# Optimization experiments

Hardware: AMD Instinct MI355X
Metric: run time of the kernel (lower is better)

The kernel has to match this reference:

```python
import jax, jax.numpy as jnp
import numpy as np
import math

C = 512
B, T = 8, 2048
STRIDE = 2
LN_EPS = 1e-5
EPS = 1e-8


def _ln(x, g, b):
    mu = jnp.mean(x, axis=-1, keepdims=True)
    var = jnp.mean(jnp.square(x - mu), axis=-1, keepdims=True)
    return (x - mu) * jax.lax.rsqrt(var + LN_EPS) * g + b


def _lin(x, w, b):
    # torch Linear: y = x @ W^T + b, W: [out, in]
    return jnp.einsum('btc,oc->bto', x, w) + b


def setup_inputs() -> dict:
    key = jax.random.key(0)
    ks = iter(jax.random.split(key, 40))
    s = 0.02
    d = {'x': jax.random.normal(next(ks), (B, T, C), jnp.float32)}
    # downsample conv: [C_out, C_in, K]
    d['dw'] = jax.random.normal(next(ks), (C, C, 3), jnp.float32) * s
    d['db'] = jnp.zeros((C,), jnp.float32)
    for br in ('cr', 'd', 'c'):
        for p in ('q', 'k', 'v'):
            d[f'w{p}_{br}'] = jax.random.normal(next(ks), (C, C), jnp.float32) * s
            d[f'b{p}_{br}'] = jnp.zeros((C,), jnp.float32)
        d[f'ln_{br}_g'] = jnp.ones((C,), jnp.float32)
        d[f'ln_{br}_b'] = jnp.zeros((C,), jnp.float32)
    d['temp'] = jnp.asarray(0.1, jnp.float32)
    d['gw'] = jax.random.normal(next(ks), (3, 3 * C), jnp.float32) * s  # conv1d k=1 squeezed
    d['gb'] = jnp.zeros((3,), jnp.float32)
    return d


def _forward(x, dw, db, wq_cr, bq_cr, wk_cr, bk_cr, wv_cr, bv_cr, ln_cr_g, ln_cr_b,
             wq_d, bq_d, wk_d, bk_d, wv_d, bv_d, ln_d_g, ln_d_b,
             wq_c, bq_c, wk_c, bk_c, wv_c, bv_c, ln_c_g, ln_c_b,
             temp, gw, gb):
    scale = 1.0 / math.sqrt(C)
    # downsample: Conv1d(k=3, stride, pad=1) on [B,C,T]
    xc = jnp.transpose(x, (0, 2, 1))
    xd = jax.lax.conv_general_dilated(
        xc, dw, window_strides=(STRIDE,), padding=[(1, 1)],
        dimension_numbers=('NCH', 'OIH', 'NCH')) + db[None, :, None]
    x_down = jnp.transpose(xd, (0, 2, 1))  # [B, T//2, C]

    # cross-resolution branch
    q = _lin(x, wq_cr, bq_cr)
    k = _lin(x_down, wk_cr, bk_cr)
    v = _lin(x_down, wv_cr, bv_cr)
    a = jax.nn.softmax(jnp.einsum('btc,bsc->bts', q, k) * scale, axis=-1)
    out_cross = _ln(jnp.einsum('bts,bsc->btc', a, v), ln_cr_g, ln_cr_b)

    # dot-product branch
    q = _lin(x, wq_d, bq_d)
    k = _lin(x, wk_d, bk_d)
    v = _lin(x, wv_d, bv_d)
    a = jax.nn.softmax(jnp.einsum('btc,bsc->bts', q, k) * scale, axis=-1)
    out_dot = _ln(jnp.einsum('bts,bsc->btc', a, v), ln_d_g, ln_d_b)

    # cosine branch with learnable temperature
    q = _lin(x, wq_c, bq_c)
    k = _lin(x, wk_c, bk_c)
    qn = q / (jnp.linalg.norm(q, axis=2, keepdims=True) + EPS)
    kn = k / (jnp.linalg.norm(k, axis=2, keepdims=True) + EPS)
    t = jnp.maximum(temp, 0.01)
    a = jax.nn.softmax(jnp.einsum('btc,bsc->bts', qn, kn) / t, axis=-1)
    v = _lin(x, wv_c, bv_c)
    out_cos = _ln(jnp.einsum('bts,bsc->btc', a, v), ln_c_g, ln_c_b)

    # learned gating fusion (conv1d k=1 == per-position linear over 3C)
    fused = jnp.concatenate([out_cross, out_dot, out_cos], axis=-1)  # [B,T,3C]
    gate = jax.nn.softmax(jnp.einsum('btc,gc->btg', fused, gw) + gb, axis=-1)  # [B,T,3]
    z = (gate[..., 0:1] * out_cross + gate[..., 1:2] * out_dot + gate[..., 2:3] * out_cos)
    return z


def reference(x, dw, db, wq_cr, bq_cr, wk_cr, bk_cr, wv_cr, bv_cr, ln_cr_g, ln_cr_b,
              wq_d, bq_d, wk_d, bk_d, wv_d, bv_d, ln_d_g, ln_d_b,
              wq_c, bq_c, wk_c, bk_c, wv_c, bv_c, ln_c_g, ln_c_b,
              temp, gw, gb):
    return _forward(x, dw, db, wq_cr, bq_cr, wk_cr, bk_cr, wv_cr, bv_cr, ln_cr_g, ln_cr_b,
                    wq_d, bq_d, wk_d, bk_d, wv_d, bv_d, ln_d_g, ln_d_b,
                    wq_c, bq_c, wk_c, bk_c, wv_c, bv_c, ln_c_g, ln_c_b,
                    temp, gw, gb)
```

## Files before the change

kernel.cpp:

```cpp
#include <hip/hip_runtime.h>


typedef __attribute__((ext_vector_type(8))) __bf16 bf16x8;
typedef __attribute__((ext_vector_type(4))) float f32x4;

#define CDIM 512
#define TFULL 2048

#define GLL16(gp, lp)                                                        \
  __builtin_amdgcn_global_load_lds(                                          \
      (const __attribute__((address_space(1))) unsigned int*)(gp),           \
      (__attribute__((address_space(3))) unsigned int*)(lp), 16, 0, 0)

__device__ __forceinline__ unsigned short f2bf(float f) {
  unsigned u = __float_as_uint(f);
  u = (u + 0x7fffu + ((u >> 16) & 1u)) >> 16;
  return (unsigned short)u;
}
__device__ __forceinline__ float bf2f(unsigned short h) {
  return __uint_as_float(((unsigned)h) << 16);
}

__global__ __launch_bounds__(256)
void k_tobf16(const float* __restrict__ src, unsigned short* __restrict__ dst, long n4) {
  long i = (long)blockIdx.x * 256 + threadIdx.x;
  if (i >= n4) return;
  float4 f = reinterpret_cast<const float4*>(src)[i];
  unsigned short o4[4] = {f2bf(f.x), f2bf(f.y), f2bf(f.z), f2bf(f.w)};
  reinterpret_cast<uint2*>(dst)[i] = *reinterpret_cast<const uint2*>(o4);
}

struct WPtrs { const float* p[9]; };
__global__ __launch_bounds__(256)
void k_tobf16w(WPtrs w, unsigned short* __restrict__ dst) {
  int idx = blockIdx.x * 256 + threadIdx.x;
  if (idx >= 9 * 65536) return;
  int m = idx >> 16, off = idx & 65535;
  float4 f = reinterpret_cast<const float4*>(w.p[m])[off];
  unsigned short o4[4] = {f2bf(f.x), f2bf(f.y), f2bf(f.z), f2bf(f.w)};
  reinterpret_cast<uint2*>(dst + (long)m * 262144)[off] = *reinterpret_cast<const uint2*>(o4);
}

__global__ __launch_bounds__(256)
void k_dwreorder(const float* __restrict__ dw, unsigned short* __restrict__ dwb) {
  int idx = blockIdx.x * 256 + threadIdx.x;
  if (idx >= 512 * 1536) return;
  int o = idx / 1536, rem = idx - o * 1536;
  int k = rem >> 9, i = rem & 511;
  dwb[idx] = f2bf(dw[(o * 512 + i) * 3 + k]);
}

__global__ __launch_bounds__(256)
void k_fix(const unsigned short* __restrict__ XB, const unsigned short* __restrict__ DWB,
           const float* __restrict__ db, unsigned short* __restrict__ XD) {
  const int lane = threadIdx.x & 63, wave = threadIdx.x >> 6;
  const int idx = blockIdx.x * 4 + wave;
  const int b = idx >> 9, o = idx & 511;
  const unsigned short* xr = XB + (long)b * TFULL * CDIM + lane * 16;
  const unsigned short* wr = DWB + (long)o * 1536 + 512 + lane * 16;
  float acc = 0.f;
  uint4 xv0 = *reinterpret_cast<const uint4*>(xr);
  uint4 xv1 = *reinterpret_cast<const uint4*>(xr + 8);
  uint4 wv0 = *reinterpret_cast<const uint4*>(wr);
  uint4 wv1 = *reinterpret_cast<const uint4*>(wr + 8);
  const unsigned short* xp0 = (const unsigned short*)&xv0;
  const unsigned short* xp1 = (const unsigned short*)&xv1;
  const unsigned short* wp0 = (const unsigned short*)&wv0;
  const unsigned short* wp1 = (const unsigned short*)&wv1;
#pragma unroll
  for (int j = 0; j < 8; ++j) acc += bf2f(xp0[j]) * bf2f(wp0[j]);
#pragma unroll
  for (int j = 0; j < 8; ++j) acc += bf2f(xp1[j]) * bf2f(wp1[j]);
#pragma unroll
  for (int off = 32; off > 0; off >>= 1) acc += __shfl_xor(acc, off);
  if (lane == 0) XD[(long)b * 1024 * 512 + o] = f2bf(acc + db[o]);
}

__global__ __launch_bounds__(256)
void k_gemm(const unsigned short* __restrict__ A,
            const unsigned short* __restrict__ B,
            void* __restrict__ Cp,
            int K, int lda, int ldb, int ldc,
            long sA, long sB, long sC,
            const float* __restrict__ bias,
            float alpha, int mode) {
  const int gx = gridDim.x;
  const int nwg = gx * gridDim.y;
  int wg = blockIdx.x + gx * blockIdx.y;
  wg = (wg & 7) * (nwg >> 3) + (wg >> 3);
  const int tm0 = (wg % gx) * 128, tn0 = (wg / gx) * 128;
  const int bz = blockIdx.z;
  const unsigned short* Ag = A + (long)bz * sA;
  const unsigned short* Bg = B + (long)bz * sB;

  __shared__ __align__(16) unsigned short smem[32768];

  const int tid = threadIdx.x;
  const int lane = tid & 63;
  const int wave = tid >> 6;
  const int wm = (wave >> 1) * 64, wn = (wave & 1) * 64;
  const int lrow = lane & 15, kq = lane >> 4;

  f32x4 acc[4][4];
#pragma unroll
  for (int i = 0; i < 4; ++i)
#pragma unroll
    for (int j = 0; j < 4; ++j) acc[i][j] = f32x4{0.f, 0.f, 0.f, 0.f};

  const int sr = tid >> 3;
  const int sj = (tid & 7) ^ (sr & 7);
  const unsigned short* aSrc = Ag + (long)(tm0 + sr) * lda + sj * 8;
  const unsigned short* bSrc = Bg + (long)(tn0 + sr) * ldb + sj * 8;

  const int nt = K >> 6;

#define STAGE(kt_, buf_)                                                     \
  {                                                                          \
    unsigned short* aD = smem + (buf_) * 8192 + wave * 512;                  \
    unsigned short* bD = smem + 16384 + (buf_) * 8192 + wave * 512;          \
    _Pragma("unroll")                                                        \
    for (int rd = 0; rd < 4; ++rd) {                                         \
      GLL16(aSrc + (kt_) + (long)rd * 32 * lda, aD + rd * 2048);             \
      GLL16(bSrc + (kt_) + (long)rd * 32 * ldb, bD + rd * 2048);             \
    }                                                                        \
  }

  STAGE(0, 0);

  const int xr = (lrow & 7) << 3;
  for (int t = 0; t < nt; ++t) {
    if (t + 1 < nt) {
      STAGE((t + 1) << 6, (t + 1) & 1);
      asm volatile("s_waitcnt vmcnt(8)" ::: "memory");
    } else {
      asm volatile("s_waitcnt vmcnt(0)" ::: "memory");
    }
    __builtin_amdgcn_s_barrier();
    __builtin_amdgcn_sched_barrier(0);
    const unsigned short* As_ = smem + (t & 1) * 8192;
    const unsigned short* Bs_ = smem + 16384 + (t & 1) * 8192;
    bf16x8 af[4][2], bfv[4][2];
#pragma unroll
    for (int mi = 0; mi < 4; ++mi)
#pragma unroll
      for (int ks = 0; ks < 2; ++ks)
        af[mi][ks] = *reinterpret_cast<const bf16x8*>(
            &As_[(wm + mi * 16 + lrow) * 64 + ((ks * 32 + kq * 8) ^ xr)]);
#pragma unroll
    for (int ni = 0; ni < 4; ++ni)
#pragma unroll
      for (int ks = 0; ks < 2; ++ks)
        bfv[ni][ks] = *reinterpret_cast<const bf16x8*>(
            &Bs_[(wn + ni * 16 + lrow) * 64 + ((ks * 32 + kq * 8) ^ xr)]);
#pragma unroll
    for (int mi = 0; mi < 4; ++mi)
#pragma unroll
      for (int ni = 0; ni < 4; ++ni) {
        acc[mi][ni] = __builtin_amdgcn_mfma_f32_16x16x32_bf16(af[mi][0], bfv[ni][0], acc[mi][ni], 0, 0, 0);
        acc[mi][ni] = __builtin_amdgcn_mfma_f32_16x16x32_bf16(af[mi][1], bfv[ni][1], acc[mi][ni], 0, 0, 0);
      }
    __builtin_amdgcn_sched_barrier(0);
    if (t + 1 < nt) __builtin_amdgcn_s_barrier();
  }
#undef STAGE

  unsigned short* Cb = (unsigned short*)Cp + (long)bz * sC;
  if (mode == 1) {
#pragma unroll
    for (int mi = 0; mi < 4; ++mi) {
      int rg = tm0 + wm + mi * 16 + kq * 4;
#pragma unroll
      for (int ni = 0; ni < 4; ++ni) {
        int cg = tn0 + wn + ni * 16 + lrow;
        float bb = bias ? bias[cg] : 0.f;
        f32x4 v = acc[mi][ni];
#pragma unroll
        for (int r = 0; r < 4; ++r)
          Cb[(long)(rg + r) * ldc + cg] = f2bf(v[r] * alpha + bb);
      }
    }
  } else {
#pragma unroll
    for (int mi = 0; mi < 4; ++mi) {
      int rg = tm0 + wm + mi * 16 + kq * 4;
      float rb[4];
#pragma unroll
      for (int r = 0; r < 4; ++r) rb[r] = bias[rg + r];
#pragma unroll
      for (int ni = 0; ni < 4; ++ni) {
        int cg = tn0 + wn + ni * 16 + lrow;
        f32x4 v = acc[mi][ni];
#pragma unroll
        for (int r = 0; r < 4; ++r)
          Cb[(long)(rg + r) * ldc + cg] = f2bf(v[r] * alpha + rb[r]);
      }
    }
  }
}

__global__ __launch_bounds__(256)
void k_gemm64(const unsigned short* __restrict__ A,
              const unsigned short* __restrict__ B,
              void* __restrict__ Cp,
              int K, int lda, int ldb, int ldc,
              long sA, long sB, long sC,
              const float* __restrict__ bias,
              float alpha, int mode) {
  const int gx = gridDim.x;
  const int nwg = gx * gridDim.y;
  int wg = blockIdx.x + gx * blockIdx.y;
  wg = (wg & 7) * (nwg >> 3) + (wg >> 3);
  const int tm0 = (wg % gx) * 128, tn0 = (wg / gx) * 64;
  const int bz = blockIdx.z;
  const unsigned short* Ag = A + (long)bz * sA;
  const unsigned short* Bg = B + (long)bz * sB;

  __shared__ __align__(16) unsigned short smem[24576];

  const int tid = threadIdx.x;
  const int lane = tid & 63;
  const int wave = tid >> 6;
  const int wm = (wave >> 1) * 64, wn = (wave & 1) * 32;
  const int lrow = lane & 15, kq = lane >> 4;

  f32x4 acc[4][2];
#pragma unroll
  for (int i = 0; i < 4; ++i)
#pragma unroll
    for (int j = 0; j < 2; ++j) acc[i][j] = f32x4{0.f, 0.f, 0.f, 0.f};

  const int sr = tid >> 3;
  const int sj = (tid & 7) ^ (sr & 7);
  const unsigned short* aSrc = Ag + (long)(tm0 + sr) * lda + sj * 8;
  const unsigned short* bSrc = Bg + (long)(tn0 + sr) * ldb + sj * 8;

  const int nt = K >> 6;

#define STAGE64(kt_, buf_)                                                   \
  {                                                                          \
    unsigned short* aD = smem + (buf_) * 8192 + wave * 512;                  \
    unsigned short* bD = smem + 16384 + (buf_) * 4096 + wave * 512;          \
    _Pragma("unroll")                                                        \
    for (int rd = 0; rd < 4; ++rd)                                           \
      GLL16(aSrc + (kt_) + (long)rd * 32 * lda, aD + rd * 2048);             \
    _Pragma("unroll")                                                        \
    for (int rd = 0; rd < 2; ++rd)                                           \
      GLL16(bSrc + (kt_) + (long)rd * 32 * ldb, bD + rd * 2048);             \
  }

  STAGE64(0, 0);

  const int xr = (lrow & 7) << 3;
  for (int t = 0; t < nt; ++t) {
    if (t + 1 < nt) {
      STAGE64((t + 1) << 6, (t + 1) & 1);
      asm volatile("s_waitcnt vmcnt(6)" ::: "memory");
    } else {
      asm volatile("s_waitcnt vmcnt(0)" ::: "memory");
    }
    __builtin_amdgcn_s_barrier();
    __builtin_amdgcn_sched_barrier(0);
    const unsigned short* As_ = smem + (t & 1) * 8192;
    const unsigned short* Bs_ = smem + 16384 + (t & 1) * 4096;
    bf16x8 af[4][2], bfv[2][2];
#pragma unroll
    for (int mi = 0; mi < 4; ++mi)
#pragma unroll
      for (int ks = 0; ks < 2; ++ks)
        af[mi][ks] = *reinterpret_cast<const bf16x8*>(
            &As_[(wm + mi * 16 + lrow) * 64 + ((ks * 32 + kq * 8) ^ xr)]);
#pragma unroll
    for (int ni = 0; ni < 2; ++ni)
#pragma unroll
      for (int ks = 0; ks < 2; ++ks)
        bfv[ni][ks] = *reinterpret_cast<const bf16x8*>(
            &Bs_[(wn + ni * 16 + lrow) * 64 + ((ks * 32 + kq * 8) ^ xr)]);
#pragma unroll
    for (int mi = 0; mi < 4; ++mi)
#pragma unroll
      for (int ni = 0; ni < 2; ++ni) {
        acc[mi][ni] = __builtin_amdgcn_mfma_f32_16x16x32_bf16(af[mi][0], bfv[ni][0], acc[mi][ni], 0, 0, 0);
        acc[mi][ni] = __builtin_amdgcn_mfma_f32_16x16x32_bf16(af[mi][1], bfv[ni][1], acc[mi][ni], 0, 0, 0);
      }
    __builtin_amdgcn_sched_barrier(0);
    if (t + 1 < nt) __builtin_amdgcn_s_barrier();
  }
#undef STAGE64

  unsigned short* Cb = (unsigned short*)Cp + (long)bz * sC;
  if (mode == 1) {
#pragma unroll
    for (int mi = 0; mi < 4; ++mi) {
      int rg = tm0 + wm + mi * 16 + kq * 4;
#pragma unroll
      for (int ni = 0; ni < 2; ++ni) {
        int cg = tn0 + wn + ni * 16 + lrow;
        float bb = bias ? bias[cg] : 0.f;
        f32x4 v = acc[mi][ni];
#pragma unroll
        for (int r = 0; r < 4; ++r)
          Cb[(long)(rg + r) * ldc + cg] = f2bf(v[r] * alpha + bb);
      }
    }
  } else {
#pragma unroll
    for (int mi = 0; mi < 4; ++mi) {
      int rg = tm0 + wm + mi * 16 + kq * 4;
      float rb[4];
#pragma unroll
      for (int r = 0; r < 4; ++r) rb[r] = bias[rg + r];
#pragma unroll
      for (int ni = 0; ni < 2; ++ni) {
        int cg = tn0 + wn + ni * 16 + lrow;
        f32x4 v = acc[mi][ni];
#pragma unroll
        for (int r = 0; r < 4; ++r)
          Cb[(long)(rg + r) * ldc + cg] = f2bf(v[r] * alpha + rb[r]);
      }
    }
  }
}

__global__ __launch_bounds__(512)
void k_gemm256(const unsigned short* __restrict__ A,
               const unsigned short* __restrict__ B,
               unsigned short* __restrict__ C,
               int K, int lda, int ldb, int ldc,
               long sA, long sB, long sC,
               float alpha, const float* __restrict__ tempPtr) {
  const int gx = gridDim.x;
  const int nwg = gx * gridDim.y;
  int wg = blockIdx.x + gx * blockIdx.y;
  wg = (wg & 7) * (nwg >> 3) + (wg >> 3);
  const int tm0 = (wg % gx) * 256, tn0 = (wg / gx) * 256;
  const unsigned short* Ag = A + (long)blockIdx.z * sA;
  const unsigned short* Bg = B + (long)blockIdx.z * sB;

  __shared__ __align__(16) unsigned short smem[32768];

  const int tid = threadIdx.x;
  const int lane = tid & 63;
  const int wave = tid >> 6;
  const int wm = (wave >> 2) * 128, wn = (wave & 3) * 64;
  const int lrow = lane & 15, kq = lane >> 4;

  f32x4 acc[8][4];
#pragma unroll
  for (int i = 0; i < 8; ++i)
#pragma unroll
    for (int j = 0; j < 4; ++j) acc[i][j] = f32x4{0.f, 0.f, 0.f, 0.f};

  const int srow = lane >> 2;
  const int sslot = (lane & 3) ^ ((lane >> 3) & 3);
  const unsigned short* aS0 = Ag + (long)(tm0 + wave * 16 + srow) * lda + sslot * 8;
  const unsigned short* aS1 = aS0 + 128L * lda;
  const unsigned short* bS0 = Bg + (long)(tn0 + wave * 16 + srow) * ldb + sslot * 8;
  const unsigned short* bS1 = bS0 + 128L * ldb;

  const int nt = K >> 5;

#define STAGE256(kt_, buf_)                                                  \
  {                                                                          \
    unsigned short* aD = smem + (buf_) * 8192 + wave * 512;                  \
    unsigned short* bD = smem + 16384 + (buf_) * 8192 + wave * 512;          \
    GLL16(aS0 + (kt_), aD);                                                  \
    GLL16(aS1 + (kt_), aD + 4096);                                           \
    GLL16(bS0 + (kt_), bD);                                                  \
    GLL16(bS1 + (kt_), bD + 4096);                                           \
  }

  STAGE256(0, 0);

  const int xr = ((lrow >> 1) & 3) << 3;
  for (int t = 0; t < nt; ++t) {
    if (t + 1 < nt) {
      STAGE256((t + 1) << 5, (t + 1) & 1);
      asm volatile("s_waitcnt vmcnt(4)" ::: "memory");
    } else {
      asm volatile("s_waitcnt vmcnt(0)" ::: "memory");
    }
    __builtin_amdgcn_s_barrier();
    __builtin_amdgcn_sched_barrier(0);
    const unsigned short* As_ = smem + (t & 1) * 8192;
    const unsigned short* Bs_ = smem + 16384 + (t & 1) * 8192;
    bf16x8 bfv[4];
#pragma unroll
    for (int ni = 0; ni < 4; ++ni)
      bfv[ni] = *reinterpret_cast<const bf16x8*>(
          &Bs_[(wn + ni * 16 + lrow) * 32 + ((kq * 8) ^ xr)]);
#pragma unroll
    for (int mi = 0; mi < 8; ++mi) {
      bf16x8 af = *reinterpret_cast<const bf16x8*>(
          &As_[(wm + mi * 16 + lrow) * 32 + ((kq * 8) ^ xr)]);
#pragma unroll
      for (int ni = 0; ni < 4; ++ni)
        acc[mi][ni] = __builtin_amdgcn_mfma_f32_16x16x32_bf16(af, bfv[ni], acc[mi][ni], 0, 0, 0);
    }
    __builtin_amdgcn_sched_barrier(0);
    if (t + 1 < nt) __builtin_amdgcn_s_barrier();
  }
#undef STAGE256

  if (tempPtr) alpha = 1.0f / fmaxf(*tempPtr, 0.01f);

  C += (long)blockIdx.z * sC;
#pragma unroll
  for (int mi = 0; mi < 8; ++mi) {
    int rg = tm0 + wm + mi * 16 + kq * 4;
#pragma unroll
    for (int ni = 0; ni < 4; ++ni) {
      int cg = tn0 + wn + ni * 16 + lrow;
      f32x4 v = acc[mi][ni];
#pragma unroll
      for (int r = 0; r < 4; ++r)
        C[(long)(rg + r) * ldc + cg] = f2bf(v[r] * alpha);
    }
  }
}

__global__ __launch_bounds__(256)
void k_softmax(unsigned short* __restrict__ S, int cols) {
  const long base = (long)blockIdx.x * cols;
  const int tid = threadIdx.x, lane = tid & 63, wave = tid >> 6;
  const int nv = cols >> 3;
  float f[8];
  float mx = -3.0e38f;
  if (tid < nv) {
    uint4 v = *reinterpret_cast<const uint4*>(S + base + tid * 8);
    const unsigned short* pv = (const unsigned short*)&v;
#pragma unroll
    for (int j = 0; j < 8; ++j) { f[j] = bf2f(pv[j]); mx = fmaxf(mx, f[j]); }
  }
  __shared__ float rmax[4], rsum[4];
#pragma unroll
  for (int o = 32; o > 0; o >>= 1) mx = fmaxf(mx, __shfl_down(mx, o));
  if (lane == 0) rmax[wave] = mx;
  __syncthreads();
  mx = fmaxf(fmaxf(rmax[0], rmax[1]), fmaxf(rmax[2], rmax[3]));
  float sum = 0.f;
  if (tid < nv) {
#pragma unroll
    for (int j = 0; j < 8; ++j) { f[j] = __expf(f[j] - mx); sum += f[j]; }
  }
#pragma unroll
  for (int o = 32; o > 0; o >>= 1) sum += __shfl_down(sum, o);
  if (lane == 0) rsum[wave] = sum;
  __syncthreads();
  const float inv = 1.0f / (rsum[0] + rsum[1] + rsum[2] + rsum[3]);
  if (tid < nv) {
    unsigned short o8[8];
#pragma unroll
    for (int j = 0; j < 8; ++j) o8[j] = f2bf(f[j] * inv);
    *reinterpret_cast<uint4*>(S + base + tid * 8) = *reinterpret_cast<const uint4*>(o8);
  }
}

__global__ __launch_bounds__(256)
void k_softmax1024(unsigned short* __restrict__ S) {
  const int tid = threadIdx.x;
  const int half = tid >> 7, ht = tid & 127;
  const int lane = tid & 63, wave = tid >> 6;
  const long base = ((long)blockIdx.x * 2 + half) * 1024;
  uint4 v = *reinterpret_cast<const uint4*>(S + base + ht * 8);
  const unsigned short* pv = (const unsigned short*)&v;
  float f[8];
  float mx = -3.0e38f;
#pragma unroll
  for (int j = 0; j < 8; ++j) { f[j] = bf2f(pv[j]); mx = fmaxf(mx, f[j]); }
  __shared__ float rmax[4], rsum[4];
#pragma unroll
  for (int o = 32; o > 0; o >>= 1) mx = fmaxf(mx, __shfl_down(mx, o));
  if (lane == 0) rmax[wave] = mx;
  __syncthreads();
  mx = fmaxf(rmax[half * 2], rmax[half * 2 + 1]);
  float sum = 0.f;
#pragma unroll
  for (int j = 0; j < 8; ++j) { f[j] = __expf(f[j] - mx); sum += f[j]; }
#pragma unroll
  for (int o = 32; o > 0; o >>= 1) sum += __shfl_down(sum, o);
  if (lane == 0) rsum[wave] = sum;
  __syncthreads();
  const float inv = 1.0f / (rsum[half * 2] + rsum[half * 2 + 1]);
  unsigned short o8[8];
#pragma unroll
  for (int j = 0; j < 8; ++j) o8[j] = f2bf(f[j] * inv);
  *reinterpret_cast<uint4*>(S + base + ht * 8) = *reinterpret_cast<const uint4*>(o8);
}

__global__ __launch_bounds__(256)
void k_l2norm(unsigned short* __restrict__ Q, int ld) {
  const int lane = threadIdx.x & 63, wave = threadIdx.x >> 6;
  const long row = (long)blockIdx.x * 4 + wave;
  unsigned short* p = Q + row * ld + lane * 8;
  uint4 v = *reinterpret_cast<const uint4*>(p);
  const unsigned short* pv = (const unsigned short*)&v;
  float f[8]; float q = 0.f;
#pragma unroll
  for (int j = 0; j < 8; ++j) { f[j] = bf2f(pv[j]); q += f[j] * f[j]; }
#pragma unroll
  for (int o = 32; o > 0; o >>= 1) q += __shfl_xor(q, o);
  float sc = 1.0f / (sqrtf(q) + 1e-8f);
  unsigned short o8[8];
#pragma unroll
  for (int j = 0; j < 8; ++j) o8[j] = f2bf(f[j] * sc);
  *reinterpret_cast<uint4*>(p) = *reinterpret_cast<const uint4*>(o8);
}

__global__ __launch_bounds__(256)
void k_ln_bf(unsigned short* __restrict__ X, const float* __restrict__ g,
             const float* __restrict__ b) {
  const int lane = threadIdx.x & 63, wave = threadIdx.x >> 6;
  const long row = (long)blockIdx.x * 4 + wave;
  unsigned short* p = X + row * CDIM + lane * 8;
  uint4 v = *reinterpret_cast<const uint4*>(p);
  const unsigned short* pv = (const unsigned short*)&v;
  float f[8];
  float s = 0.f, q = 0.f;
#pragma unroll
  for (int j = 0; j < 8; ++j) { f[j] = bf2f(pv[j]); s += f[j]; q += f[j] * f[j]; }
#pragma unroll
  for (int o = 32; o > 0; o >>= 1) { s += __shfl_xor(s, o); q += __shfl_xor(q, o); }
  float mu = s * (1.f / 512.f);
  float var = q * (1.f / 512.f) - mu * mu;
  float rs = rsqrtf(var + 1e-5f);
  float gg[8], bb[8];
  *reinterpret_cast<float4*>(&gg[0]) = *reinterpret_cast<const float4*>(g + lane * 8);
  *reinterpret_cast<float4*>(&gg[4]) = *reinterpret_cast<const float4*>(g + lane * 8 + 4);
  *reinterpret_cast<float4*>(&bb[0]) = *reinterpret_cast<const float4*>(b + lane * 8);
  *reinterpret_cast<float4*>(&bb[4]) = *reinterpret_cast<const float4*>(b + lane * 8 + 4);
  unsigned short o8[8];
#pragma unroll
  for (int j = 0; j < 8; ++j) o8[j] = f2bf((f[j] - mu) * rs * gg[j] + bb[j]);
  *reinterpret_cast<uint4*>(p) = *reinterpret_cast<const uint4*>(o8);
}

__global__ __launch_bounds__(256)
void k_gate(const unsigned short* __restrict__ o0, const unsigned short* __restrict__ o1,
            const unsigned short* __restrict__ o2, const float* __restrict__ gw,
            const float* __restrict__ gb, float* __restrict__ out) {
  __shared__ float gws[3 * 1536];
  for (int i = threadIdx.x; i < 3 * 1536; i += 256) gws[i] = gw[i];
  __syncthreads();
  const int lane = threadIdx.x & 63, wave = threadIdx.x >> 6;
  const long pos = (long)blockIdx.x * 4 + wave;
  const long off = pos * CDIM + lane * 8;
  float a[8], bq[8], cq[8];
  {
    uint4 va = *reinterpret_cast<const uint4*>(o0 + off);
    uint4 vb = *reinterpret_cast<const uint4*>(o1 + off);
    uint4 vc = *reinterpret_cast<const uint4*>(o2 + off);
    const unsigned short* pa = (const unsigned short*)&va;
    const unsigned short* pb = (const unsigned short*)&vb;
    const unsigned short* pc = (const unsigned short*)&vc;
#pragma unroll
    for (int j = 0; j < 8; ++j) { a[j] = bf2f(pa[j]); bq[j] = bf2f(pb[j]); cq[j] = bf2f(pc[j]); }
  }
  float l0 = 0.f, l1 = 0.f, l2 = 0.f;
  const int ch = lane * 8;
#pragma unroll
  for (int j = 0; j < 8; ++j) {
    l0 += a[j] * gws[ch + j] + bq[j] * gws[512 + ch + j] + cq[j] * gws[1024 + ch + j];
    l1 += a[j] * gws[1536 + ch + j] + bq[j] * gws[2048 + ch + j] + cq[j] * gws[2560 + ch + j];
    l2 += a[j] * gws[3072 + ch + j] + bq[j] * gws[3584 + ch + j] + cq[j] * gws[4096 + ch + j];
  }
#pragma unroll
  for (int o = 32; o > 0; o >>= 1) {
    l0 += __shfl_xor(l0, o); l1 += __shfl_xor(l1, o); l2 += __shfl_xor(l2, o);
  }
  l0 += gb[0]; l1 += gb[1]; l2 += gb[2];
  float m = fmaxf(l0, fmaxf(l1, l2));
  float e0 = __expf(l0 - m), e1 = __expf(l1 - m), e2 = __expf(l2 - m);
  float inv = 1.f / (e0 + e1 + e2);
  float g0 = e0 * inv, g1 = e1 * inv, g2 = e2 * inv;
  float r[8];
#pragma unroll
  for (int j = 0; j < 8; ++j) r[j] = g0 * a[j] + g1 * bq[j] + g2 * cq[j];
  *reinterpret_cast<float4*>(out + off) = *reinterpret_cast<const float4*>(&r[0]);
  *reinterpret_cast<float4*>(out + off + 4) = *reinterpret_cast<const float4*>(&r[4]);
}

extern "C" void kernel_launch(void* const* d_in, const int* in_sizes, int n_in,
                              void* d_out, int out_size, void* d_ws, size_t ws_size,
                              hipStream_t stream) {
  (void)in_sizes; (void)n_in; (void)out_size;
  const float* x = (const float*)d_in[0];
  const float* dw = (const float*)d_in[1];
  const float* db = (const float*)d_in[2];
  WPtrs wp;
  wp.p[0] = (const float*)d_in[3];
  wp.p[1] = (const float*)d_in[11];
  wp.p[2] = (const float*)d_in[13];
  wp.p[3] = (const float*)d_in[19];
  wp.p[4] = (const float*)d_in[21];
  wp.p[5] = (const float*)d_in[15];
  wp.p[6] = (const float*)d_in[23];
  wp.p[7] = (const float*)d_in[5];
  wp.p[8] = (const float*)d_in[7];
  const float* bq_cr = (const float*)d_in[4];
  const float* bk_cr = (const float*)d_in[6];
  const float* bv_cr = (const float*)d_in[8];
  const float* ln_cr_g = (const float*)d_in[9];
  const float* ln_cr_b = (const float*)d_in[10];
  const float* bq_d = (const float*)d_in[12];
  const float* bk_d = (const float*)d_in[14];
  const float* bv_d = (const float*)d_in[16];
  const float* ln_d_g = (const float*)d_in[17];
  const float* ln_d_b = (const float*)d_in[18];
  const float* bq_c = (const float*)d_in[20];
  const float* bk_c = (const float*)d_in[22];
  const float* bv_c = (const float*)d_in[24];
  const float* ln_c_g = (const float*)d_in[25];
  const float* ln_c_b = (const float*)d_in[26];
  const float* temp = (const float*)d_in[27];
  const float* gw = (const float*)d_in[28];
  const float* gb = (const float*)d_in[29];

  if (ws_size < 240000000ULL) return;

  char* p = (char*)d_ws;
  auto alloc = [&](size_t bytes) {
    void* r = (void*)p;
    p += (bytes + 255) & ~(size_t)255;
    return r;
  };
  alloc(1024);
  unsigned short* XB  = (unsigned short*)alloc(16384L * 512 * 2);
  unsigned short* XD  = (unsigned short*)alloc(8192L * 512 * 2);
  unsigned short* WB  = (unsigned short*)alloc(9L * 262144 * 2);
  unsigned short* DWB = (unsigned short*)alloc(512L * 1536 * 2);
  unsigned short* QB  = (unsigned short*)alloc(16384L * 512 * 2);
  unsigned short* KB  = (unsigned short*)alloc(8192L * 512 * 2);
  unsigned short* VT  = (unsigned short*)alloc(512L * 16384 * 2);
  unsigned short* OUT0 = (unsigned short*)alloc(16384L * 512 * 2);
  unsigned short* OUT1 = (unsigned short*)alloc(16384L * 512 * 2);
  unsigned short* OUT2 = (unsigned short*)alloc(16384L * 512 * 2);
  unsigned short* QK2 = (unsigned short*)alloc(16384L * 1024 * 2);
  float* BC = (float*)alloc(2048 * 4);
  unsigned short* SB = (unsigned short*)alloc(8L * 2048 * 2048 * 2);

  const float scale = 0.044194173824159216f;

  auto gemm = [&](const unsigned short* A, const unsigned short* Bm, void* Cm,
                  int M, int N, int K, int lda, int ldb, int ldc,
                  int batch, long sA, long sB, long sC,
                  const float* bias, float alpha, int mode) {
    dim3 g(M / 128, N / 128, batch);
    k_gemm<<<g, 256, 0, stream>>>(A, Bm, Cm, K, lda, ldb, ldc, sA, sB, sC,
                                  bias, alpha, mode);
  };
  auto gemm64 = [&](const unsigned short* A, const unsigned short* Bm, void* Cm,
                    int M, int N, int K, int lda, int ldb, int ldc,
                    int batch, long sA, long sB, long sC,
                    const float* bias, float alpha, int mode) {
    dim3 g(M / 128, N / 64, batch);
    k_gemm64<<<g, 256, 0, stream>>>(A, Bm, Cm, K, lda, ldb, ldc, sA, sB, sC,
                                    bias, alpha, mode);
  };
  auto gemm256 = [&](const unsigned short* A, const unsigned short* Bm,
                     unsigned short* Cm, int M, int N, int K,
                     int lda, int ldb, int ldc, int batch,
                     long sA, long sB, long sC, float alpha, const float* tp) {
    dim3 g(M / 256, N / 256, batch);
    k_gemm256<<<g, 512, 0, stream>>>(A, Bm, Cm, K, lda, ldb, ldc, sA, sB, sC, alpha, tp);
  };

  k_tobf16<<<8192, 256, 0, stream>>>(x, XB, 16384L * 512 / 4);
  k_tobf16w<<<2304, 256, 0, stream>>>(wp, WB);
  k_dwreorder<<<3072, 256, 0, stream>>>(dw, DWB);
  hipMemcpyAsync(BC,        bq_d, 512 * 4, hipMemcpyDeviceToDevice, stream);
  hipMemcpyAsync(BC + 512,  bk_d, 512 * 4, hipMemcpyDeviceToDevice, stream);
  hipMemcpyAsync(BC + 1024, bq_c, 512 * 4, hipMemcpyDeviceToDevice, stream);
  hipMemcpyAsync(BC + 1536, bk_c, 512 * 4, hipMemcpyDeviceToDevice, stream);

  gemm(XB - 512, DWB, XD, 1024, 512, 1536, 1024, 1536, 512,
       8, 1048576L, 0, 524288L, db, 1.f, 1);
  k_fix<<<1024, 256, 0, stream>>>(XB, DWB, db, XD);

  gemm(XB, WB + 0 * 262144L, QB, 16384, 512, 512, 512, 512, 512, 1, 0, 0, 0,
       bq_cr, 1.f, 1);
  gemm(XD, WB + 7 * 262144L, KB, 8192, 512, 512, 512, 512, 512, 1, 0, 0, 0,
       bk_cr, 1.f, 1);
  gemm64(WB + 8 * 262144L, XD, VT, 512, 8192, 512, 512, 512, 8192, 1, 0, 0, 0,
         bv_cr, 1.f, 3);
  gemm256(QB, KB, SB, 2048, 1024, 512, 512, 512, 1024, 8,
          2048L * 512, 1024L * 512, 2048L * 1024, scale, nullptr);
  k_softmax1024<<<8192, 256, 0, stream>>>(SB);
  gemm(SB, VT, OUT0, 2048, 512, 1024, 1024, 8192, 512, 8,
       2048L * 1024, 1024, 2048L * 512, nullptr, 1.f, 1);
  k_ln_bf<<<4096, 256, 0, stream>>>(OUT0, ln_cr_g, ln_cr_b);

  gemm(XB, WB + 1 * 262144L, QK2, 16384, 1024, 512, 512, 512, 1024, 1, 0, 0, 0,
       BC, 1.f, 1);
  gemm64(WB + 5 * 262144L, XB, VT, 512, 16384, 512, 512, 512, 16384, 1, 0, 0, 0,
         bv_d, 1.f, 3);
  gemm256(QK2, QK2 + 512, SB, 2048, 2048, 512, 1024, 1024, 2048, 8,
          2048L * 1024, 2048L * 1024, 2048L * 2048, scale, nullptr);
  k_softmax<<<16384, 256, 0, stream>>>(SB, 2048);
  gemm(SB, VT, OUT1, 2048, 512, 2048, 2048, 16384, 512, 8,
       2048L * 2048, 2048, 2048L * 512, nullptr, 1.f, 1);
  k_ln_bf<<<4096, 256, 0, stream>>>(OUT1, ln_d_g, ln_d_b);

  gemm(XB, WB + 3 * 262144L, QK2, 16384, 1024, 512, 512, 512, 1024, 1, 0, 0, 0,
       BC + 1024, 1.f, 1);
  k_l2norm<<<4096, 256, 0, stream>>>(QK2, 1024);
  k_l2norm<<<4096, 256, 0, stream>>>(QK2 + 512, 1024);
  gemm64(WB + 6 * 262144L, XB, VT, 512, 16384, 512, 512, 512, 16384, 1, 0, 0, 0,
         bv_c, 1.f, 3);
  gemm256(QK2, QK2 + 512, SB, 2048, 2048, 512, 1024, 1024, 2048, 8,
          2048L * 1024, 2048L * 1024, 2048L * 2048, 1.f, temp);
  k_softmax<<<16384, 256, 0, stream>>>(SB, 2048);
  gemm(SB, VT, OUT2, 2048, 512, 2048, 2048, 16384, 512, 8,
       2048L * 2048, 2048, 2048L * 512, nullptr, 1.f, 1);
  k_ln_bf<<<4096, 256, 0, stream>>>(OUT2, ln_c_g, ln_c_b);

  k_gate<<<4096, 256, 0, stream>>>(OUT0, OUT1, OUT2, gw, gb, (float*)d_out);
}
```

Measured before the change: 546.3 us.

## Fuse LayerNorms into gate kernel, merge l2norm launches, use 64-tile GEMMs for small problems

The three separate LayerNorm passes are folded into the gating kernel, which now normalizes each branch output in registers before computing gate logits. This removes three read/write round trips over the branch outputs and three launches. The two l2norm launches become one kernel over both halves of the Q/K buffer. The downsample conv GEMM and the cross-branch K projection switch to the 64-tile GEMM variant, presumably for better occupancy on these smaller problems. As a side effect, LayerNorm outputs are no longer rounded to bf16 before gating.

```diff
diff --git a/kernel.cpp b/kernel.cpp
--- a/kernel.cpp
+++ b/kernel.cpp
@@ -488,10 +488,10 @@
 }
 
 __global__ __launch_bounds__(256)
-void k_l2norm(unsigned short* __restrict__ Q, int ld) {
+void k_l2norm2(unsigned short* __restrict__ Q) {
   const int lane = threadIdx.x & 63, wave = threadIdx.x >> 6;
-  const long row = (long)blockIdx.x * 4 + wave;
-  unsigned short* p = Q + row * ld + lane * 8;
+  const int idx = blockIdx.x * 4 + wave;
+  unsigned short* p = Q + (long)(idx >> 1) * 1024 + (idx & 1) * 512 + lane * 8;
   uint4 v = *reinterpret_cast<const uint4*>(p);
   const unsigned short* pv = (const unsigned short*)&v;
   float f[8]; float q = 0.f;
@@ -507,37 +507,13 @@
 }
 
 __global__ __launch_bounds__(256)
-void k_ln_bf(unsigned short* __restrict__ X, const float* __restrict__ g,
-             const float* __restrict__ b) {
-  const int lane = threadIdx.x & 63, wave = threadIdx.x >> 6;
-  const long row = (long)blockIdx.x * 4 + wave;
-  unsigned short* p = X + row * CDIM + lane * 8;
-  uint4 v = *reinterpret_cast<const uint4*>(p);
-  const unsigned short* pv = (const unsigned short*)&v;
-  float f[8];
-  float s = 0.f, q = 0.f;
-#pragma unroll
-  for (int j = 0; j < 8; ++j) { f[j] = bf2f(pv[j]); s += f[j]; q += f[j] * f[j]; }
-#pragma unroll
-  for (int o = 32; o > 0; o >>= 1) { s += __shfl_xor(s, o); q += __shfl_xor(q, o); }
-  float mu = s * (1.f / 512.f);
-  float var = q * (1.f / 512.f) - mu * mu;
-  float rs = rsqrtf(var + 1e-5f);
-  float gg[8], bb[8];
-  *reinterpret_cast<float4*>(&gg[0]) = *reinterpret_cast<const float4*>(g + lane * 8);
-  *reinterpret_cast<float4*>(&gg[4]) = *reinterpret_cast<const float4*>(g + lane * 8 + 4);
-  *reinterpret_cast<float4*>(&bb[0]) = *reinterpret_cast<const float4*>(b + lane * 8);
-  *reinterpret_cast<float4*>(&bb[4]) = *reinterpret_cast<const float4*>(b + lane * 8 + 4);
-  unsigned short o8[8];
-#pragma unroll
-  for (int j = 0; j < 8; ++j) o8[j] = f2bf((f[j] - mu) * rs * gg[j] + bb[j]);
-  *reinterpret_cast<uint4*>(p) = *reinterpret_cast<const uint4*>(o8);
-}
-
-__global__ __launch_bounds__(256)
 void k_gate(const unsigned short* __restrict__ o0, const unsigned short* __restrict__ o1,
             const unsigned short* __restrict__ o2, const float* __restrict__ gw,
-            const float* __restrict__ gb, float* __restrict__ out) {
+            const float* __restrict__ gb,
+            const float* __restrict__ g0, const float* __restrict__ b0,
+            const float* __restrict__ g1, const float* __restrict__ b1,
+            const float* __restrict__ g2, const float* __restrict__ b2,
+            float* __restrict__ out) {
   __shared__ float gws[3 * 1536];
   for (int i = threadIdx.x; i < 3 * 1536; i += 256) gws[i] = gw[i];
   __syncthreads();
@@ -555,8 +531,44 @@
 #pragma unroll
     for (int j = 0; j < 8; ++j) { a[j] = bf2f(pa[j]); bq[j] = bf2f(pb[j]); cq[j] = bf2f(pc[j]); }
   }
+  float sa = 0.f, qa = 0.f, sb = 0.f, qb = 0.f, sc2 = 0.f, qc = 0.f;
+#pragma unroll
+  for (int j = 0; j < 8; ++j) {
+    sa += a[j];  qa += a[j] * a[j];
+    sb += bq[j]; qb += bq[j] * bq[j];
+    sc2 += cq[j]; qc += cq[j] * cq[j];
+  }
+#pragma unroll
+  for (int o = 32; o > 0; o >>= 1) {
+    sa += __shfl_xor(sa, o);  qa += __shfl_xor(qa, o);
+    sb += __shfl_xor(sb, o);  qb += __shfl_xor(qb, o);
+    sc2 += __shfl_xor(sc2, o); qc += __shfl_xor(qc, o);
+  }
+  const float inv512 = 1.f / 512.f;
+  float mua = sa * inv512, rsa = rsqrtf(qa * inv512 - mua * mua + 1e-5f);
+  float mub = sb * inv512, rsb = rsqrtf(qb * inv512 - mub * mub + 1e-5f);
+  float muc = sc2 * inv512, rsc = rsqrtf(qc * inv512 - muc * muc + 1e-5f);
+  const int ch = lane * 8;
+  float gga[8], bba[8], ggb[8], bbb[8], ggc[8], bbc[8];
+  *reinterpret_cast<float4*>(&gga[0]) = *reinterpret_cast<const float4*>(g0 + ch);
+  *reinterpret_cast<float4*>(&gga[4]) = *reinterpret_cast<const float4*>(g0 + ch + 4);
+  *reinterpret_cast<float4*>(&bba[0]) = *reinterpret_cast<const float4*>(b0 + ch);
+  *reinterpret_cast<float4*>(&bba[4]) = *reinterpret_cast<const float4*>(b0 + ch + 4);
+  *reinterpret_cast<float4*>(&ggb[0]) = *reinterpret_cast<const float4*>(g1 + ch);
+  *reinterpret_cast<float4*>(&ggb[4]) = *reinterpret_cast<const float4*>(g1 + ch + 4);
+  *reinterpret_cast<float4*>(&bbb[0]) = *reinterpret_cast<const float4*>(b1 + ch);
+  *reinterpret_cast<float4*>(&bbb[4]) = *reinterpret_cast<const float4*>(b1 + ch + 4);
+  *reinterpret_cast<float4*>(&ggc[0]) = *reinterpret_cast<const float4*>(g2 + ch);
+  *reinterpret_cast<float4*>(&ggc[4]) = *reinterpret_cast<const float4*>(g2 + ch + 4);
+  *reinterpret_cast<float4*>(&bbc[0]) = *reinterpret_cast<const float4*>(b2 + ch);
+  *reinterpret_cast<float4*>(&bbc[4]) = *reinterpret_cast<const float4*>(b2 + ch + 4);
+#pragma unroll
+  for (int j = 0; j < 8; ++j) {
+    a[j]  = (a[j] - mua) * rsa * gga[j] + bba[j];
+    bq[j] = (bq[j] - mub) * rsb * ggb[j] + bbb[j];
+    cq[j] = (cq[j] - muc) * rsc * ggc[j] + bbc[j];
+  }
   float l0 = 0.f, l1 = 0.f, l2 = 0.f;
-  const int ch = lane * 8;
 #pragma unroll
   for (int j = 0; j < 8; ++j) {
     l0 += a[j] * gws[ch + j] + bq[j] * gws[512 + ch + j] + cq[j] * gws[1024 + ch + j];
@@ -571,10 +583,10 @@
   float m = fmaxf(l0, fmaxf(l1, l2));
   float e0 = __expf(l0 - m), e1 = __expf(l1 - m), e2 = __expf(l2 - m);
   float inv = 1.f / (e0 + e1 + e2);
-  float g0 = e0 * inv, g1 = e1 * inv, g2 = e2 * inv;
+  float w0 = e0 * inv, w1 = e1 * inv, w2 = e2 * inv;
   float r[8];
 #pragma unroll
-  for (int j = 0; j < 8; ++j) r[j] = g0 * a[j] + g1 * bq[j] + g2 * cq[j];
+  for (int j = 0; j < 8; ++j) r[j] = w0 * a[j] + w1 * bq[j] + w2 * cq[j];
   *reinterpret_cast<float4*>(out + off) = *reinterpret_cast<const float4*>(&r[0]);
   *reinterpret_cast<float4*>(out + off + 4) = *reinterpret_cast<const float4*>(&r[4]);
 }
@@ -672,14 +684,14 @@
   hipMemcpyAsync(BC + 1024, bq_c, 512 * 4, hipMemcpyDeviceToDevice, stream);
   hipMemcpyAsync(BC + 1536, bk_c, 512 * 4, hipMemcpyDeviceToDevice, stream);
 
-  gemm(XB - 512, DWB, XD, 1024, 512, 1536, 1024, 1536, 512,
-       8, 1048576L, 0, 524288L, db, 1.f, 1);
+  gemm64(XB - 512, DWB, XD, 1024, 512, 1536, 1024, 1536, 512,
+         8, 1048576L, 0, 524288L, db, 1.f, 1);
   k_fix<<<1024, 256, 0, stream>>>(XB, DWB, db, XD);
 
   gemm(XB, WB + 0 * 262144L, QB, 16384, 512, 512, 512, 512, 512, 1, 0, 0, 0,
        bq_cr, 1.f, 1);
-  gemm(XD, WB + 7 * 262144L, KB, 8192, 512, 512, 512, 512, 512, 1, 0, 0, 0,
-       bk_cr, 1.f, 1);
+  gemm64(XD, WB + 7 * 262144L, KB, 8192, 512, 512, 512, 512, 512, 1, 0, 0, 0,
+         bk_cr, 1.f, 1);
   gemm64(WB + 8 * 262144L, XD, VT, 512, 8192, 512, 512, 512, 8192, 1, 0, 0, 0,
          bv_cr, 1.f, 3);
   gemm256(QB, KB, SB, 2048, 1024, 512, 512, 512, 1024, 8,
@@ -687,7 +699,6 @@
   k_softmax1024<<<8192, 256, 0, stream>>>(SB);
   gemm(SB, VT, OUT0, 2048, 512, 1024, 1024, 8192, 512, 8,
        2048L * 1024, 1024, 2048L * 512, nullptr, 1.f, 1);
-  k_ln_bf<<<4096, 256, 0, stream>>>(OUT0, ln_cr_g, ln_cr_b);
 
   gemm(XB, WB + 1 * 262144L, QK2, 16384, 1024, 512, 512, 512, 1024, 1, 0, 0, 0,
        BC, 1.f, 1);
@@ -698,12 +709,10 @@
   k_softmax<<<16384, 256, 0, stream>>>(SB, 2048);
   gemm(SB, VT, OUT1, 2048, 512, 2048, 2048, 16384, 512, 8,
        2048L * 2048, 2048, 2048L * 512, nullptr, 1.f, 1);
-  k_ln_bf<<<4096, 256, 0, stream>>>(OUT1, ln_d_g, ln_d_b);
 
   gemm(XB, WB + 3 * 262144L, QK2, 16384, 1024, 512, 512, 512, 1024, 1, 0, 0, 0,
        BC + 1024, 1.f, 1);
-  k_l2norm<<<4096, 256, 0, stream>>>(QK2, 1024);
-  k_l2norm<<<4096, 256, 0, stream>>>(QK2 + 512, 1024);
+  k_l2norm2<<<8192, 256, 0, stream>>>(QK2);
   gemm64(WB + 6 * 262144L, XB, VT, 512, 16384, 512, 512, 512, 16384, 1, 0, 0, 0,
          bv_c, 1.f, 3);
   gemm256(QK2, QK2 + 512, SB, 2048, 2048, 512, 1024, 1024, 2048, 8,
@@ -711,7 +720,8 @@
   k_softmax<<<16384, 256, 0, stream>>>(SB, 2048);
   gemm(SB, VT, OUT2, 2048, 512, 2048, 2048, 16384, 512, 8,
        2048L * 2048, 2048, 2048L * 512, nullptr, 1.f, 1);
-  k_ln_bf<<<4096, 256, 0, stream>>>(OUT2, ln_c_g, ln_c_b);
-
-  k_gate<<<4096, 256, 0, stream>>>(OUT0, OUT1, OUT2, gw, gb, (float*)d_out);
-}
+
+  k_gate<<<4096, 256, 0, stream>>>(OUT0, OUT1, OUT2, gw, gb,
+                                   ln_cr_g, ln_cr_b, ln_d_g, ln_d_b,
+                                   ln_c_g, ln_c_b, (float*)d_out);
+}
```

New measurement: 539.8 us. About the same (-1.2%).
